# Kernel optimization log

Hardware: AMD Instinct MI355X
Metric: run time of the kernel (lower is better)

## Reference

```python
import jax, jax.numpy as jnp
import numpy as np

B, C, H, W = 8, 128, 64, 64


def setup_inputs() -> dict:
    key = jax.random.key(0)
    ks = jax.random.split(key, 4)
    s = 1.0 / np.sqrt(C)
    return {
        "x": jax.random.normal(ks[0], (B, C, H, W), dtype=jnp.float32),
        "Wq": jax.random.normal(ks[1], (C, C), dtype=jnp.float32) * s,
        "bq": jnp.zeros((C,), dtype=jnp.float32),
        "Wk": jax.random.normal(ks[2], (C, C), dtype=jnp.float32) * s,
        "bk": jnp.zeros((C,), dtype=jnp.float32),
        "Wv": jax.random.normal(ks[3], (C, C), dtype=jnp.float32) * s,
        "bv": jnp.zeros((C,), dtype=jnp.float32),
    }


def reference(x, Wq, bq, Wk, bk, Wv, bv):
    b, c, h, w = x.shape
    xf = x.reshape(b, c, h * w)  # [B, C, N]
    # 1x1 convs are per-pixel CxC matmuls (weight[out,in] contracted over in)
    q = jnp.einsum("oc,bcn->bon", Wq, xf) + bq[None, :, None]
    k = jnp.einsum("oc,bcn->bon", Wk, xf) + bk[None, :, None]
    v = jnp.einsum("oc,bcn->bon", Wv, xf) + bv[None, :, None]
    scale = 1.0 / jnp.sqrt(jnp.asarray(c, dtype=x.dtype))
    attn = jnp.einsum("bcn,bcm->bnm", q, k) * scale  # [B, N, N]
    attn = jax.nn.softmax(attn, axis=-1)
    out = jnp.einsum("bnm,bcm->bcn", attn, v)  # [B, C, N]
    return out.reshape(b, c, h, w) + x
```

## Files before the change

kernel.cpp:

```cpp
#include <hip/hip_runtime.h>

#define B_ 8
#define C_ 128
#define N_ 4096
#define SCALE 0.08838834764831845f

typedef __attribute__((ext_vector_type(8))) short short8;
typedef __attribute__((ext_vector_type(4))) short short4v;
typedef __attribute__((ext_vector_type(4))) float f32x4;

__device__ inline float b2f(unsigned short u) {
    union { unsigned int i; float f; } v; v.i = ((unsigned int)u) << 16; return v.f;
}
__device__ inline unsigned short f2b(float f) {
    unsigned int x = __float_as_uint(f);
    return (unsigned short)((x + 0x7FFFu + ((x >> 16) & 1u)) >> 16);
}

__device__ inline void gld_lds16(const void* g, void* l) {
    __builtin_amdgcn_global_load_lds(
        (const __attribute__((address_space(1))) unsigned int*)g,
        (__attribute__((address_space(3))) unsigned int*)l, 16, 0, 0);
}

__global__ __launch_bounds__(256) void qkv_mfma(
    const float* __restrict__ x,
    const float* __restrict__ Wq, const float* __restrict__ bq,
    const float* __restrict__ Wk, const float* __restrict__ bk,
    const float* __restrict__ Wv, const float* __restrict__ bv,
    float* __restrict__ q, unsigned short* __restrict__ kTs,
    unsigned short* __restrict__ vS)
{
    __shared__ __align__(16) short Xs[64 * 128];
    __shared__ __align__(16) float Obuf[128 * 68];

    const int t    = threadIdx.x;
    const int w    = t >> 6;
    const int lane = t & 63;
    const int l15  = lane & 15;
    const int quad = lane >> 4;

    const int b  = blockIdx.x & 7;
    const int n0 = (blockIdx.x >> 3) * 64;
    const long base = (long)b * C_ * N_;

    #pragma unroll
    for (int it = 0; it < 8; ++it) {
        const int c  = (t >> 4) + it * 16;
        const int n4 = (t & 15) * 4;
        const float4 xv = *(const float4*)(const void*)(x + base + (long)c * N_ + n0 + n4);
        const int bc = c >> 3, cl = c & 7;
        Xs[(n4 + 0) * 128 + ((bc ^ ((n4 + 0) & 15)) << 3) + cl] = (short)f2b(xv.x);
        Xs[(n4 + 1) * 128 + ((bc ^ ((n4 + 1) & 15)) << 3) + cl] = (short)f2b(xv.y);
        Xs[(n4 + 2) * 128 + ((bc ^ ((n4 + 2) & 15)) << 3) + cl] = (short)f2b(xv.z);
        Xs[(n4 + 3) * 128 + ((bc ^ ((n4 + 3) & 15)) << 3) + cl] = (short)f2b(xv.w);
    }
    __syncthreads();

    auto gemm = [&](const float* __restrict__ W, const float* __restrict__ bias,
                    f32x4 (&acc)[2][4]) {
        short8 af[2][4];
        #pragma unroll
        for (int ot = 0; ot < 2; ++ot) {
            const int o = 32 * w + 16 * ot + l15;
            #pragma unroll
            for (int ks = 0; ks < 4; ++ks) {
                const float4 a0 = *(const float4*)(const void*)(W + o * C_ + ks * 32 + quad * 8);
                const float4 a1 = *(const float4*)(const void*)(W + o * C_ + ks * 32 + quad * 8 + 4);
                short8 f;
                f[0] = (short)f2b(a0.x); f[1] = (short)f2b(a0.y);
                f[2] = (short)f2b(a0.z); f[3] = (short)f2b(a0.w);
                f[4] = (short)f2b(a1.x); f[5] = (short)f2b(a1.y);
                f[6] = (short)f2b(a1.z); f[7] = (short)f2b(a1.w);
                af[ot][ks] = f;
            }
        }
        #pragma unroll
        for (int ot = 0; ot < 2; ++ot)
            #pragma unroll
            for (int nt = 0; nt < 4; ++nt)
                acc[ot][nt] = (f32x4){0.f, 0.f, 0.f, 0.f};
        #pragma unroll
        for (int nt = 0; nt < 4; ++nt) {
            const int n = nt * 16 + l15;
            short8 bx[4];
            #pragma unroll
            for (int ks = 0; ks < 4; ++ks)
                bx[ks] = *(const short8*)(const void*)(Xs + n * 128 + (((ks * 4 + quad) ^ l15) << 3));
            #pragma unroll
            for (int ot = 0; ot < 2; ++ot)
                #pragma unroll
                for (int ks = 0; ks < 4; ++ks)
                    acc[ot][nt] = __builtin_amdgcn_mfma_f32_16x16x32_bf16(af[ot][ks], bx[ks], acc[ot][nt], 0, 0, 0);
        }
        #pragma unroll
        for (int ot = 0; ot < 2; ++ot) {
            #pragma unroll
            for (int r = 0; r < 4; ++r) {
                const float bb = bias[32 * w + 16 * ot + quad * 4 + r];
                #pragma unroll
                for (int nt = 0; nt < 4; ++nt) acc[ot][nt][r] += bb;
            }
        }
    };

    {
        f32x4 acc[2][4];
        gemm(Wq, bq, acc);
        #pragma unroll
        for (int ot = 0; ot < 2; ++ot)
            #pragma unroll
            for (int nt = 0; nt < 4; ++nt)
                #pragma unroll
                for (int r = 0; r < 4; ++r)
                    Obuf[(32 * w + 16 * ot + quad * 4 + r) * 68 + nt * 16 + l15] = acc[ot][nt][r];
        __syncthreads();
        const int o = t >> 1, nh = (t & 1) * 32;
        #pragma unroll
        for (int i = 0; i < 32; i += 4)
            *(float4*)(void*)(q + base + (long)o * N_ + n0 + nh + i) =
                *(const float4*)(const void*)(Obuf + o * 68 + nh + i);
        __syncthreads();
    }

    {
        f32x4 acc[2][4];
        gemm(Wk, bk, acc);
        #pragma unroll
        for (int ot = 0; ot < 2; ++ot)
            #pragma unroll
            for (int nt = 0; nt < 4; ++nt)
                #pragma unroll
                for (int r = 0; r < 4; ++r) {
                    const int o = 32 * w + 16 * ot + quad * 4 + r;
                    Obuf[(nt * 16 + l15) * 128 + (((o >> 3) ^ l15) << 3) + (o & 7)] = acc[ot][nt][r];
                }
        __syncthreads();
        const int n = t >> 2, oh = (t & 3) * 32;
        #pragma unroll
        for (int i = 0; i < 32; i += 4) {
            const float4 kv = *(const float4*)(const void*)(Obuf + n * 128 + oh + i);
            short4v s;
            s[0] = (short)f2b(kv.x); s[1] = (short)f2b(kv.y);
            s[2] = (short)f2b(kv.z); s[3] = (short)f2b(kv.w);
            *(short4v*)(void*)(kTs + base + (long)(n0 + n) * C_ + oh + i) = s;
        }
        __syncthreads();
    }

    {
        f32x4 acc[2][4];
        gemm(Wv, bv, acc);
        #pragma unroll
        for (int ot = 0; ot < 2; ++ot)
            #pragma unroll
            for (int nt = 0; nt < 4; ++nt)
                #pragma unroll
                for (int r = 0; r < 4; ++r) {
                    const int o = 32 * w + 16 * ot + quad * 4 + r;
                    const int n = nt * 16 + l15;
                    Obuf[o * 64 + (n & 32) + ((((n >> 3) & 3) ^ ((o >> 1) & 3)) << 3) + (n & 7)] = acc[ot][nt][r];
                }
        __syncthreads();
        const int o = t >> 1, nh = (t & 1) * 32;
        #pragma unroll
        for (int i = 0; i < 32; i += 4) {
            const float4 vv = *(const float4*)(const void*)(Obuf + o * 64 + nh + i);
            short4v s;
            s[0] = (short)f2b(vv.x); s[1] = (short)f2b(vv.y);
            s[2] = (short)f2b(vv.z); s[3] = (short)f2b(vv.w);
            *(short4v*)(void*)(vS + base + (long)o * N_ + n0 + nh + i) = s;
        }
    }
}

__global__ __launch_bounds__(512) void attn_mfma(
    const float* qg,
    const unsigned short* __restrict__ kTs,
    const unsigned short* __restrict__ vS,
    const float* __restrict__ xg,
    float* out)
{
    __shared__ union {
        struct {
            short K[2][2][4096];
            short V[2][2][4096];
            short Pb[8][16 * 40];
        } s;
        float Ot[64 * 130];
    } sm;
    __shared__ float Ls[2][4][16];
    __shared__ float linvA[64];

    const int t    = threadIdx.x;
    const int w    = t >> 6;
    const int g    = w >> 2;
    const int wq   = w & 3;
    const int lane = t & 63;
    const int l15  = lane & 15;
    const int quad = lane >> 4;

    const int b  = blockIdx.x & 7;
    const int n0 = (blockIdx.x >> 3) * 64;
    const long base = (long)b * C_ * N_;

    const int query = n0 + 16 * wq + l15;
    short8 qf[4];
    #pragma unroll
    for (int ks = 0; ks < 4; ++ks) {
        short8 f;
        #pragma unroll
        for (int j = 0; j < 8; ++j) {
            const int c = ks * 32 + quad * 8 + j;
            f[j] = (short)f2b(qg[base + (long)c * N_ + query]);
        }
        qf[ks] = f;
    }

    f32x4 acc[8];
    #pragma unroll
    for (int ct = 0; ct < 8; ++ct) acc[ct] = (f32x4){0.f, 0.f, 0.f, 0.f};
    f32x4 accS = (f32x4){0.f, 0.f, 0.f, 0.f};
    short8 ones;
    #pragma unroll
    for (int j = 0; j < 8; ++j) ones[j] = (short)0x3F80;

    auto stage = [&](int buf, int pair) {
        const int mt = pair * 2 + g;
        const char* gK = (const char*)(kTs + base + (long)mt * 32 * C_);
        char* lK = (char*)sm.s.K[buf][g];
        char* lV = (char*)sm.s.V[buf][g];
        #pragma unroll
        for (int jj = 0; jj < 2; ++jj) {
            const int d = wq * 2048 + jj * 1024;
            gld_lds16(gK + d + lane * 16, lK + d);
            const int dv = d + lane * 16;
            const int c  = dv >> 6;
            gld_lds16((const char*)(vS + base + (long)c * N_ + mt * 32) + (dv & 63), lV + d);
        }
    };

    auto compute = [&](int buf) {
        const short* Kb = sm.s.K[buf][g];
        const short* Vb = sm.s.V[buf][g];
        f32x4 sc[2];
        sc[0] = (f32x4){0.f, 0.f, 0.f, 0.f};
        sc[1] = (f32x4){0.f, 0.f, 0.f, 0.f};
        #pragma unroll
        for (int kt = 0; kt < 2; ++kt) {
            const int row = (kt * 16 + l15) * 128;
            #pragma unroll
            for (int ks = 0; ks < 4; ++ks) {
                const short8 kf = *(const short8*)(const void*)(Kb + row + (((ks * 4 + quad) ^ l15) << 3));
                sc[kt] = __builtin_amdgcn_mfma_f32_16x16x32_bf16(qf[ks], kf, sc[kt], 0, 0, 0);
            }
        }
        short* Pw = sm.s.Pb[w];
        #pragma unroll
        for (int kt = 0; kt < 2; ++kt)
            #pragma unroll
            for (int r = 0; r < 4; ++r)
                Pw[(quad * 4 + r) * 40 + kt * 16 + l15] = (short)f2b(__expf(sc[kt][r] * SCALE));
        const short8 pf = *(const short8*)(const void*)(Pw + l15 * 40 + quad * 8);
        accS = __builtin_amdgcn_mfma_f32_16x16x32_bf16(pf, ones, accS, 0, 0, 0);
        #pragma unroll
        for (int ct = 0; ct < 8; ++ct) {
            const short8 vf = *(const short8*)(const void*)(Vb + (ct * 16 + l15) * 32 + ((quad ^ ((l15 >> 1) & 3)) << 3));
            acc[ct] = __builtin_amdgcn_mfma_f32_16x16x32_bf16(pf, vf, acc[ct], 0, 0, 0);
        }
    };

    stage(0, 0);
    __syncthreads();
    for (int i = 0; i < 64; ++i) {
        if (i < 63) stage((i + 1) & 1, i + 1);
        compute(i & 1);
        __syncthreads();
    }

    if (l15 == 0) {
        #pragma unroll
        for (int r = 0; r < 4; ++r) Ls[g][wq][quad * 4 + r] = accS[r];
    }
    if (g == 0) {
        #pragma unroll
        for (int ct = 0; ct < 8; ++ct)
            #pragma unroll
            for (int r = 0; r < 4; ++r)
                sm.Ot[(16 * wq + quad * 4 + r) * 130 + ct * 16 + l15] = acc[ct][r];
    }
    __syncthreads();
    if (g == 1) {
        #pragma unroll
        for (int ct = 0; ct < 8; ++ct)
            #pragma unroll
            for (int r = 0; r < 4; ++r)
                sm.Ot[(16 * wq + quad * 4 + r) * 130 + ct * 16 + l15] += acc[ct][r];
    } else if (l15 == 0) {
        #pragma unroll
        for (int r = 0; r < 4; ++r) {
            const int row = 16 * wq + quad * 4 + r;
            linvA[row] = 1.0f / fmaxf(Ls[0][wq][quad * 4 + r] + Ls[1][wq][quad * 4 + r], 1e-20f);
        }
    }
    __syncthreads();

    const int c  = t >> 2;
    const int nh = (t & 3) * 16;
    const long gb = base + (long)c * N_ + n0 + nh;
    #pragma unroll
    for (int i = 0; i < 16; i += 4) {
        const float4 xs = *(const float4*)(const void*)(xg + gb + i);
        float4 rv;
        rv.x = sm.Ot[(nh + i + 0) * 130 + c] * linvA[nh + i + 0] + xs.x;
        rv.y = sm.Ot[(nh + i + 1) * 130 + c] * linvA[nh + i + 1] + xs.y;
        rv.z = sm.Ot[(nh + i + 2) * 130 + c] * linvA[nh + i + 2] + xs.z;
        rv.w = sm.Ot[(nh + i + 3) * 130 + c] * linvA[nh + i + 3] + xs.w;
        *(float4*)(void*)(out + gb + i) = rv;
    }
}

extern "C" void kernel_launch(void* const* d_in, const int* in_sizes, int n_in,
                              void* d_out, int out_size, void* d_ws, size_t ws_size,
                              hipStream_t stream) {
    const float* x  = (const float*)d_in[0];
    const float* Wq = (const float*)d_in[1];
    const float* bq = (const float*)d_in[2];
    const float* Wk = (const float*)d_in[3];
    const float* bk = (const float*)d_in[4];
    const float* Wv = (const float*)d_in[5];
    const float* bv = (const float*)d_in[6];
    float* out = (float*)d_out;

    const long BCN = (long)B_ * C_ * N_;
    unsigned short* kTs = (unsigned short*)d_ws;
    unsigned short* vS  = kTs + BCN;

    qkv_mfma<<<512, 256, 0, stream>>>(x, Wq, bq, Wk, bk, Wv, bv, out, kTs, vS);
    attn_mfma<<<B_ * (N_ / 64), 512, 0, stream>>>(out, kTs, vS, x, out);
}
```

Before: 206.2 us.

## Prefetch next weight fragments during QKV GEMMs and write Q/V directly

The QKV projection kernel now loads and converts the next weight matrix into registers while the current MFMA pass runs. Q and V are stored straight from accumulators to global memory instead of being staged through LDS, which removes several barriers. The softmax scale is folded into Q so the attention inner loop drops one multiply per score. The trade-offs are higher register pressure and narrower, less coalesced scalar global stores for Q and V.

```diff
diff --git a/kernel.cpp b/kernel.cpp
--- a/kernel.cpp
+++ b/kernel.cpp
@@ -32,7 +32,7 @@
     unsigned short* __restrict__ vS)
 {
     __shared__ __align__(16) short Xs[64 * 128];
-    __shared__ __align__(16) float Obuf[128 * 68];
+    __shared__ __align__(16) float Obuf[64 * 132];
 
     const int t    = threadIdx.x;
     const int w    = t >> 6;
@@ -43,6 +43,48 @@
     const int b  = blockIdx.x & 7;
     const int n0 = (blockIdx.x >> 3) * 64;
     const long base = (long)b * C_ * N_;
+
+    auto load_af = [&](const float* __restrict__ W, short8 (&af)[2][4]) {
+        #pragma unroll
+        for (int ot = 0; ot < 2; ++ot) {
+            const int o = 32 * w + 16 * ot + l15;
+            #pragma unroll
+            for (int ks = 0; ks < 4; ++ks) {
+                const float4 a0 = *(const float4*)(const void*)(W + o * C_ + ks * 32 + quad * 8);
+                const float4 a1 = *(const float4*)(const void*)(W + o * C_ + ks * 32 + quad * 8 + 4);
+                short8 f;
+                f[0] = (short)f2b(a0.x); f[1] = (short)f2b(a0.y);
+                f[2] = (short)f2b(a0.z); f[3] = (short)f2b(a0.w);
+                f[4] = (short)f2b(a1.x); f[5] = (short)f2b(a1.y);
+                f[6] = (short)f2b(a1.z); f[7] = (short)f2b(a1.w);
+                af[ot][ks] = f;
+            }
+        }
+    };
+
+    auto mfma_pass = [&](const short8 (&af)[2][4], f32x4 (&acc)[2][4]) {
+        #pragma unroll
+        for (int ot = 0; ot < 2; ++ot)
+            #pragma unroll
+            for (int nt = 0; nt < 4; ++nt)
+                acc[ot][nt] = (f32x4){0.f, 0.f, 0.f, 0.f};
+        #pragma unroll
+        for (int nt = 0; nt < 4; ++nt) {
+            const int n = nt * 16 + l15;
+            short8 bx[4];
+            #pragma unroll
+            for (int ks = 0; ks < 4; ++ks)
+                bx[ks] = *(const short8*)(const void*)(Xs + n * 128 + (((ks * 4 + quad) ^ l15) << 3));
+            #pragma unroll
+            for (int ot = 0; ot < 2; ++ot)
+                #pragma unroll
+                for (int ks = 0; ks < 4; ++ks)
+                    acc[ot][nt] = __builtin_amdgcn_mfma_f32_16x16x32_bf16(af[ot][ks], bx[ks], acc[ot][nt], 0, 0, 0);
+        }
+    };
+
+    short8 afA[2][4], afB[2][4];
+    load_af(Wq, afA);
 
     #pragma unroll
     for (int it = 0; it < 8; ++it) {
@@ -57,119 +99,66 @@
     }
     __syncthreads();
 
-    auto gemm = [&](const float* __restrict__ W, const float* __restrict__ bias,
-                    f32x4 (&acc)[2][4]) {
-        short8 af[2][4];
-        #pragma unroll
-        for (int ot = 0; ot < 2; ++ot) {
-            const int o = 32 * w + 16 * ot + l15;
-            #pragma unroll
-            for (int ks = 0; ks < 4; ++ks) {
-                const float4 a0 = *(const float4*)(const void*)(W + o * C_ + ks * 32 + quad * 8);
-                const float4 a1 = *(const float4*)(const void*)(W + o * C_ + ks * 32 + quad * 8 + 4);
-                short8 f;
-                f[0] = (short)f2b(a0.x); f[1] = (short)f2b(a0.y);
-                f[2] = (short)f2b(a0.z); f[3] = (short)f2b(a0.w);
-                f[4] = (short)f2b(a1.x); f[5] = (short)f2b(a1.y);
-                f[6] = (short)f2b(a1.z); f[7] = (short)f2b(a1.w);
-                af[ot][ks] = f;
-            }
-        }
+    {
+        load_af(Wv, afB);
+        f32x4 acc[2][4];
+        mfma_pass(afA, acc);
         #pragma unroll
         for (int ot = 0; ot < 2; ++ot)
             #pragma unroll
-            for (int nt = 0; nt < 4; ++nt)
-                acc[ot][nt] = (f32x4){0.f, 0.f, 0.f, 0.f};
-        #pragma unroll
-        for (int nt = 0; nt < 4; ++nt) {
-            const int n = nt * 16 + l15;
-            short8 bx[4];
-            #pragma unroll
-            for (int ks = 0; ks < 4; ++ks)
-                bx[ks] = *(const short8*)(const void*)(Xs + n * 128 + (((ks * 4 + quad) ^ l15) << 3));
-            #pragma unroll
-            for (int ot = 0; ot < 2; ++ot)
+            for (int r = 0; r < 4; ++r) {
+                const int o = 32 * w + 16 * ot + quad * 4 + r;
+                const float bb = bq[o];
                 #pragma unroll
-                for (int ks = 0; ks < 4; ++ks)
-                    acc[ot][nt] = __builtin_amdgcn_mfma_f32_16x16x32_bf16(af[ot][ks], bx[ks], acc[ot][nt], 0, 0, 0);
-        }
-        #pragma unroll
-        for (int ot = 0; ot < 2; ++ot) {
+                for (int nt = 0; nt < 4; ++nt)
+                    q[base + (long)o * N_ + n0 + nt * 16 + l15] = (acc[ot][nt][r] + bb) * SCALE;
+            }
+    }
+
+    {
+        load_af(Wk, afA);
+        f32x4 acc[2][4];
+        mfma_pass(afB, acc);
+        #pragma unroll
+        for (int ot = 0; ot < 2; ++ot)
             #pragma unroll
             for (int r = 0; r < 4; ++r) {
-                const float bb = bias[32 * w + 16 * ot + quad * 4 + r];
+                const int o = 32 * w + 16 * ot + quad * 4 + r;
+                const float bb = bv[o];
+                const int sw = ((o >> 1) & 3) << 3;
                 #pragma unroll
-                for (int nt = 0; nt < 4; ++nt) acc[ot][nt][r] += bb;
-            }
-        }
-    };
+                for (int nt = 0; nt < 4; ++nt) {
+                    const int n = nt * 16 + l15;
+                    const int ns = (n & 32) | ((((n >> 3) & 3) << 3) ^ sw) | (n & 7);
+                    vS[base + (long)o * N_ + n0 + ns] = f2b(acc[ot][nt][r] + bb);
+                }
+            }
+    }
 
     {
         f32x4 acc[2][4];
-        gemm(Wq, bq, acc);
+        mfma_pass(afA, acc);
         #pragma unroll
         for (int ot = 0; ot < 2; ++ot)
             #pragma unroll
-            for (int nt = 0; nt < 4; ++nt)
+            for (int r = 0; r < 4; ++r) {
+                const int o = 32 * w + 16 * ot + quad * 4 + r;
+                const float bb = bk[o];
                 #pragma unroll
-                for (int r = 0; r < 4; ++r)
-                    Obuf[(32 * w + 16 * ot + quad * 4 + r) * 68 + nt * 16 + l15] = acc[ot][nt][r];
-        __syncthreads();
-        const int o = t >> 1, nh = (t & 1) * 32;
-        #pragma unroll
-        for (int i = 0; i < 32; i += 4)
-            *(float4*)(void*)(q + base + (long)o * N_ + n0 + nh + i) =
-                *(const float4*)(const void*)(Obuf + o * 68 + nh + i);
-        __syncthreads();
-    }
-
-    {
-        f32x4 acc[2][4];
-        gemm(Wk, bk, acc);
-        #pragma unroll
-        for (int ot = 0; ot < 2; ++ot)
-            #pragma unroll
-            for (int nt = 0; nt < 4; ++nt)
-                #pragma unroll
-                for (int r = 0; r < 4; ++r) {
-                    const int o = 32 * w + 16 * ot + quad * 4 + r;
-                    Obuf[(nt * 16 + l15) * 128 + (((o >> 3) ^ l15) << 3) + (o & 7)] = acc[ot][nt][r];
+                for (int nt = 0; nt < 4; ++nt) {
+                    const int n = nt * 16 + l15;
+                    Obuf[n * 132 + (((o >> 3) ^ l15) << 3) + (o & 7)] = acc[ot][nt][r] + bb;
                 }
+            }
         __syncthreads();
         const int n = t >> 2, oh = (t & 3) * 32;
         #pragma unroll
         for (int i = 0; i < 32; i += 4) {
-            const float4 kv = *(const float4*)(const void*)(Obuf + n * 128 + oh + i);
+            const float4 kv = *(const float4*)(const void*)(Obuf + n * 132 + oh + i);
             short4v s;
             s[0] = (short)f2b(kv.x); s[1] = (short)f2b(kv.y);
             s[2] = (short)f2b(kv.z); s[3] = (short)f2b(kv.w);
             *(short4v*)(void*)(kTs + base + (long)(n0 + n) * C_ + oh + i) = s;
-        }
-        __syncthreads();
-    }
-
-    {
-        f32x4 acc[2][4];
-        gemm(Wv, bv, acc);
-        #pragma unroll
-        for (int ot = 0; ot < 2; ++ot)
-            #pragma unroll
-            for (int nt = 0; nt < 4; ++nt)
-                #pragma unroll
-                for (int r = 0; r < 4; ++r) {
-                    const int o = 32 * w + 16 * ot + quad * 4 + r;
-                    const int n = nt * 16 + l15;
-                    Obuf[o * 64 + (n & 32) + ((((n >> 3) & 3) ^ ((o >> 1) & 3)) << 3) + (n & 7)] = acc[ot][nt][r];
-                }
-        __syncthreads();
-        const int o = t >> 1, nh = (t & 1) * 32;
-        #pragma unroll
-        for (int i = 0; i < 32; i += 4) {
-            const float4 vv = *(const float4*)(const void*)(Obuf + o * 64 + nh + i);
-            short4v s;
-            s[0] = (short)f2b(vv.x); s[1] = (short)f2b(vv.y);
-            s[2] = (short)f2b(vv.z); s[3] = (short)f2b(vv.w);
-            *(short4v*)(void*)(vS + base + (long)o * N_ + n0 + nh + i) = s;
         }
     }
 }
@@ -260,7 +249,7 @@
         for (int kt = 0; kt < 2; ++kt)
             #pragma unroll
             for (int r = 0; r < 4; ++r)
-                Pw[(quad * 4 + r) * 40 + kt * 16 + l15] = (short)f2b(__expf(sc[kt][r] * SCALE));
+                Pw[(quad * 4 + r) * 40 + kt * 16 + l15] = (short)f2b(__expf(sc[kt][r]));
         const short8 pf = *(const short8*)(const void*)(Pw + l15 * 40 + quad * 8);
         accS = __builtin_amdgcn_mfma_f32_16x16x32_bf16(pf, ones, accS, 0, 0, 0);
         #pragma unroll
```

Result: faster. 198.7 us (-3.6%).
